# Kernel tuning notes

Hardware: AMD Instinct MI355X
Metric: run time of the kernel (lower is better)

The kernel has to match this reference:

```python
import jax, jax.numpy as jnp
import numpy as np

N = 100000   # num_entities
R = 474      # num_relations (already doubled for inverses)
D = 256      # in_dim == out_dim
E = 1000000  # num edges (first half 'in' mode, second half 'out' mode)
BN_EPS = 1e-5


def setup_inputs() -> dict:
    key = jax.random.key(0)
    ks = jax.random.split(key, 12)
    s = 1.0 / np.sqrt(D)
    return {
        "x": jax.random.normal(ks[0], (N, D), jnp.float32),
        "r": jax.random.normal(ks[1], (R, D), jnp.float32),
        "w_in": jax.random.normal(ks[2], (D, D), jnp.float32) * s,
        "w_out": jax.random.normal(ks[3], (D, D), jnp.float32) * s,
        "w_loop": jax.random.normal(ks[4], (D, D), jnp.float32) * s,
        "w_rel": jax.random.normal(ks[5], (D, D), jnp.float32) * s,
        "loop_rel": jax.random.normal(ks[6], (1, D), jnp.float32),
        "bias": jnp.zeros((D,), jnp.float32),
        "bn_gamma": jnp.ones((D,), jnp.float32),
        "bn_beta": jnp.zeros((D,), jnp.float32),
        "edge_index": jax.random.randint(ks[7], (2, E), 0, N, jnp.int32),
        "edge_type": jax.random.randint(ks[8], (E,), 0, R, jnp.int32),
    }


def reference(x, r, w_in, w_out, w_loop, w_rel, loop_rel, bias,
              bn_gamma, bn_beta, edge_index, edge_type):
    row, col = edge_index[0], edge_index[1]
    # symmetric edge norm 1/(sqrt(D_i) sqrt(D_j)); degrees over all edges
    deg = jax.ops.segment_sum(jnp.ones((E,), x.dtype), row, num_segments=N)
    deg_inv = jnp.where(deg > 0, deg ** -0.5, 0.0)
    norm = deg_inv[row] * deg_inv[col]  # [E]

    r_full = jnp.concatenate([r, loop_rel], axis=0)  # [R+1, D]

    def mode_agg(rw, cl, et, nrm, W):
        # gather -> composition (sub) -> per-mode matmul -> edge-norm -> scatter-add
        composed = x[cl] - r_full[et]                  # [e, D]
        msg = (composed @ W) * nrm[:, None]            # [e, D]
        return jax.ops.segment_sum(msg, rw, num_segments=N)

    half = edge_type.shape[0] // 2
    agg_in = mode_agg(row[:half], col[:half], edge_type[:half], norm[:half], w_in)
    agg_out = mode_agg(row[half:], col[half:], edge_type[half:], norm[half:], w_out)
    # self-loop: every node, relation = loop_rel (no edge norm)
    agg_loop = (x - loop_rel) @ w_loop                 # [N, D]

    h = agg_in + agg_out + agg_loop + bias
    # BatchNorm1d over node dim (batch statistics)
    mean = jnp.mean(h, axis=0)
    var = jnp.var(h, axis=0)
    h = bn_gamma * (h - mean) * jax.lax.rsqrt(var + BN_EPS) + bn_beta
    h = jnp.tanh(h)

    r_out = r @ w_rel  # rel_transformation == 'linear'
    return h, r_out
```

## Files before the change

### kernel.cpp

```cpp
#include <hip/hip_runtime.h>
#include <hip/hip_bf16.h>
#include <stdint.h>

#define D_DIM 256
#define KBIG 768

typedef __attribute__((ext_vector_type(8))) short bf16x8_t;
typedef __attribute__((ext_vector_type(4))) float f32x4_t;
typedef __attribute__((ext_vector_type(2))) float f32x2_t;

__device__ __forceinline__ float bf2f(uint16_t u) {
    union { uint32_t i; float f; } v; v.i = ((uint32_t)u) << 16; return v.f;
}
__device__ __forceinline__ uint16_t f2bf(float f) {
    union { float f; uint32_t i; } v; v.f = f;
    uint32_t x = v.i;
    uint32_t r = (x + 0x7FFFu + ((x >> 16) & 1u)) >> 16;
    return (uint16_t)r;
}
__device__ __forceinline__ uint32_t pack2(float a, float b) {
    return (uint32_t)f2bf(a) | ((uint32_t)f2bf(b) << 16);
}
__device__ __forceinline__ float loadv(const void* base, int f, size_t idx) {
    return f ? ((const float*)base)[idx] : bf2f(((const uint16_t*)base)[idx]);
}
__device__ __forceinline__ float fast_tanh(float x) {
    float t = __builtin_amdgcn_exp2f(x * 2.8853900817779268f);
    return 1.f - 2.f * __builtin_amdgcn_rcpf(t + 1.f);
}
__device__ __forceinline__ f32x2_t up2(uint32_t w) {
    union { uint32_t u[2]; f32x2_t f; } c;
    c.u[0] = w << 16;
    c.u[1] = w & 0xFFFF0000u;
    return c.f;
}
__device__ __forceinline__ void pkfma(f32x2_t& acc, f32x2_t a, f32x2_t b) {
    asm("v_pk_fma_f32 %0, %1, %2, %0" : "+v"(acc) : "v"(a), "v"(b));
}

__device__ __forceinline__ void gll16(const uint16_t* g, uint16_t* l) {
    __builtin_amdgcn_global_load_lds(
        (const __attribute__((address_space(1))) uint32_t*)(const void*)g,
        (__attribute__((address_space(3))) uint32_t*)(void*)l, 16, 0, 0);
}

__global__ void k_detect(const uint32_t* __restrict__ xw, int* __restrict__ flag) {
    __shared__ int cnt[256];
    int t = threadIdx.x;
    int c = 0;
    for (int j = 0; j < 16; j++) {
        uint32_t w = xw[(size_t)(t * 16 + j) * 797];
        uint32_t e = (w >> 7) & 0xFF;
        if (e >= 100 && e <= 140) c++;
    }
    cnt[t] = c;
    __syncthreads();
    for (int off = 128; off > 0; off >>= 1) {
        if (t < off) cnt[t] += cnt[t + off];
        __syncthreads();
    }
    if (t == 0) flag[0] = (cnt[0] < 2048) ? 1 : 0;
}

__global__ __launch_bounds__(256) void k_cast(const void* __restrict__ src,
                                              uint16_t* __restrict__ dst,
                                              int nvec, const int* __restrict__ flagp,
                                              int skip_bf) {
    int f = *flagp;
    int i = blockIdx.x * 256 + threadIdx.x;
    if (i >= nvec) return;
    size_t base = (size_t)i * 8;
    if (f) {
        const float* s = (const float*)src + base;
        float4 a = *(const float4*)s;
        float4 b = *(const float4*)(s + 4);
        uint4 o;
        o.x = (uint32_t)f2bf(a.x) | ((uint32_t)f2bf(a.y) << 16);
        o.y = (uint32_t)f2bf(a.z) | ((uint32_t)f2bf(a.w) << 16);
        o.z = (uint32_t)f2bf(b.x) | ((uint32_t)f2bf(b.y) << 16);
        o.w = (uint32_t)f2bf(b.z) | ((uint32_t)f2bf(b.w) << 16);
        *(uint4*)(dst + base) = o;
    } else {
        if (skip_bf) return;
        *(uint4*)(dst + base) = *(const uint4*)((const uint16_t*)src + base);
    }
}

__global__ void k_transpose(const void* __restrict__ w0, const void* __restrict__ w1,
                            const void* __restrict__ w2, const void* __restrict__ w3,
                            const int* __restrict__ flagp,
                            uint16_t* __restrict__ bt_big, uint16_t* __restrict__ bt_rel) {
    __shared__ uint16_t tile[32][33];
    int f = *flagp;
    int mat = blockIdx.z;
    const void* src = mat == 0 ? w0 : mat == 1 ? w1 : mat == 2 ? w2 : w3;
    int k0 = blockIdx.y * 32, n0 = blockIdx.x * 32;
    int tx = threadIdx.x, ty = threadIdx.y;
    tile[ty][tx] = f2bf(loadv(src, f, (size_t)(k0 + ty) * D_DIM + n0 + tx));
    __syncthreads();
    int n = n0 + ty, k = k0 + tx;
    if (mat < 3) bt_big[(size_t)n * KBIG + mat * D_DIM + k] = tile[tx][ty];
    else         bt_rel[(size_t)n * D_DIM + k] = tile[tx][ty];
}

__global__ void k_cvec(const void* __restrict__ loop_rel, const void* __restrict__ w_loop,
                       const void* __restrict__ bias, const int* __restrict__ flagp,
                       float* __restrict__ cvec) {
    int f = *flagp;
    int c = blockIdx.x;
    int lane = threadIdx.x;
    float s = 0.f;
#pragma unroll
    for (int kk = 0; kk < 4; kk++) {
        int k = kk * 64 + lane;
        s += loadv(loop_rel, f, k) * loadv(w_loop, f, (size_t)k * D_DIM + c);
    }
#pragma unroll
    for (int off = 32; off; off >>= 1) s += __shfl_down(s, off);
    if (lane == 0) cvec[c] = loadv(bias, f, c) - s;
}

__global__ void k_hist(const int* __restrict__ rows, int E, int half,
                       int* __restrict__ deg) {
    int i = blockIdx.x * blockDim.x + threadIdx.x;
    if (i < E) atomicAdd(&deg[rows[i]], (i < half) ? 0x10001 : 1);
}

__global__ void k_scan_a(const int* __restrict__ deg, int N, int* __restrict__ row_start,
                         int* __restrict__ blk_sum, float* __restrict__ dinv) {
    __shared__ int s[1024];
    int t = threadIdx.x;
    int i = blockIdx.x * 1024 + t;
    int v = (i < N) ? (deg[i] & 0xFFFF) : 0;
    if (i < N) dinv[i] = v > 0 ? rsqrtf((float)v) : 0.f;
    s[t] = v;
    __syncthreads();
    for (int off = 1; off < 1024; off <<= 1) {
        int add = (t >= off) ? s[t - off] : 0;
        __syncthreads();
        s[t] += add;
        __syncthreads();
    }
    if (i < N) row_start[i] = s[t] - v;
    if (t == 1023) blk_sum[blockIdx.x] = s[1023];
}

__global__ void k_scan_b(int* __restrict__ blk_sum, int nb) {
    __shared__ int s[128];
    int t = threadIdx.x;
    int v = (t < nb) ? blk_sum[t] : 0;
    s[t] = v;
    __syncthreads();
    for (int off = 1; off < 128; off <<= 1) {
        int add = (t >= off) ? s[t - off] : 0;
        __syncthreads();
        s[t] += add;
        __syncthreads();
    }
    if (t < nb) blk_sum[t] = s[t] - v;
}

__global__ void k_scan_c(int* __restrict__ row_start, const int* __restrict__ blk_sum,
                         const int* __restrict__ degp,
                         int N, int E, int* __restrict__ cur_in, int* __restrict__ cur_out) {
    int i = blockIdx.x * 1024 + threadIdx.x;
    if (i < N) {
        int v = row_start[i] + blk_sum[blockIdx.x];
        row_start[i] = v;
        cur_in[i] = v;
        cur_out[i] = v + (int)(((unsigned)degp[i]) >> 16);
    }
    if (i == 0) row_start[N] = E;
}

__global__ void k_fill(const int* __restrict__ ei, const int* __restrict__ et, int E, int half,
                       int* __restrict__ cur_in, int* __restrict__ cur_out,
                       const float* __restrict__ dinv, uint2* __restrict__ csr) {
    int e = blockIdx.x * blockDim.x + threadIdx.x;
    if (e >= E) return;
    int r_ = ei[e];
    int c_ = ei[E + e];
    int t_ = et[e];
    float w = dinv[r_] * dinv[c_];
    uint32_t m = ((uint32_t)c_ << 9) | (uint32_t)t_;
    int pos = (e < half) ? atomicAdd(&cur_in[r_], 1) : atomicAdd(&cur_out[r_], 1);
    csr[pos] = make_uint2(m, __float_as_uint(w));
}

__global__ __launch_bounds__(256) void k_agg(
    const uint2* __restrict__ csr, const int* __restrict__ row_start,
    const int* __restrict__ degp,
    const void* __restrict__ x_raw, const uint16_t* __restrict__ x_bf,
    const uint16_t* __restrict__ r_bf, const int* __restrict__ flagp,
    uint16_t* __restrict__ s_in, uint16_t* __restrict__ s_out, int N) {
    const char* xb = (const char*)((*flagp) ? x_bf : (const uint16_t*)x_raw);
    const char* rb = (const char*)r_bf;
    int node = blockIdx.x * 4 + (threadIdx.x >> 6);
    int lane = threadIdx.x & 63;
    if (node >= N) return;
    int half = lane >> 5;
    int cob = (lane & 31) * 16;
    int s = row_start[node], e = row_start[node + 1];
    int mid = s + (int)(((unsigned)degp[node]) >> 16);

    f32x2_t ax[4], ar[4];
    float a[8];

#pragma unroll
    for (int k = 0; k < 4; k++) { ax[k] = (f32x2_t){0.f, 0.f}; ar[k] = (f32x2_t){0.f, 0.f}; }
    for (int j = s + half; j < mid; j += 2) {
        uint2 rec = csr[j];
        uint32_t m = rec.x;
        float w = __uint_as_float(rec.y);
        uint4 xv = *(const uint4*)(xb + (m & 0xFFFFFE00u) + cob);
        uint4 rv = *(const uint4*)(rb + ((m & 511u) << 9) + cob);
        f32x2_t w2 = {w, w};
        pkfma(ax[0], up2(xv.x), w2); pkfma(ar[0], up2(rv.x), w2);
        pkfma(ax[1], up2(xv.y), w2); pkfma(ar[1], up2(rv.y), w2);
        pkfma(ax[2], up2(xv.z), w2); pkfma(ar[2], up2(rv.z), w2);
        pkfma(ax[3], up2(xv.w), w2); pkfma(ar[3], up2(rv.w), w2);
    }
#pragma unroll
    for (int k = 0; k < 4; k++) { a[2 * k] = ax[k][0] - ar[k][0]; a[2 * k + 1] = ax[k][1] - ar[k][1]; }
#pragma unroll
    for (int k = 0; k < 8; k++) a[k] += __shfl_xor(a[k], 32);
    if (half == 0) {
        uint4 o;
        o.x = pack2(a[0], a[1]); o.y = pack2(a[2], a[3]);
        o.z = pack2(a[4], a[5]); o.w = pack2(a[6], a[7]);
        *(uint4*)(s_in + (size_t)node * D_DIM + (cob >> 1)) = o;
    }

#pragma unroll
    for (int k = 0; k < 4; k++) { ax[k] = (f32x2_t){0.f, 0.f}; ar[k] = (f32x2_t){0.f, 0.f}; }
    for (int j = mid + half; j < e; j += 2) {
        uint2 rec = csr[j];
        uint32_t m = rec.x;
        float w = __uint_as_float(rec.y);
        uint4 xv = *(const uint4*)(xb + (m & 0xFFFFFE00u) + cob);
        uint4 rv = *(const uint4*)(rb + ((m & 511u) << 9) + cob);
        f32x2_t w2 = {w, w};
        pkfma(ax[0], up2(xv.x), w2); pkfma(ar[0], up2(rv.x), w2);
        pkfma(ax[1], up2(xv.y), w2); pkfma(ar[1], up2(rv.y), w2);
        pkfma(ax[2], up2(xv.z), w2); pkfma(ar[2], up2(rv.z), w2);
        pkfma(ax[3], up2(xv.w), w2); pkfma(ar[3], up2(rv.w), w2);
    }
#pragma unroll
    for (int k = 0; k < 4; k++) { a[2 * k] = ax[k][0] - ar[k][0]; a[2 * k + 1] = ax[k][1] - ar[k][1]; }
#pragma unroll
    for (int k = 0; k < 8; k++) a[k] += __shfl_xor(a[k], 32);
    if (half == 1) {
        uint4 o;
        o.x = pack2(a[0], a[1]); o.y = pack2(a[2], a[3]);
        o.z = pack2(a[4], a[5]); o.w = pack2(a[6], a[7]);
        *(uint4*)(s_out + (size_t)node * D_DIM + (cob >> 1)) = o;
    }
}

__global__ __launch_bounds__(512) void k_gemm(
    const uint16_t* a0, const uint16_t* a1,
    const uint16_t* a2, const uint16_t* a2alt, const int* __restrict__ flagp,
    int M, const uint16_t* __restrict__ bt, int bstride, int ktot,
    const float* __restrict__ addvec, uint16_t* out,
    float* __restrict__ bn_sum, float* __restrict__ bn_sq) {
    __shared__ uint16_t As[128 * 32];
    __shared__ uint16_t Bs[256 * 32];
    const uint16_t* a2s = (*flagp) ? a2 : a2alt;
    int t = threadIdx.x;
    int mbase = blockIdx.x * 128;
    int wave = t >> 6, lane = t & 63;
    int wm = (wave >> 2) * 64, wn = (wave & 3) * 64;
    int quad = lane >> 4, l15 = lane & 15;

    int roff = lane >> 2, cidx = lane & 3;
    int arowL = wave * 16 + roff;
    int achk = cidx ^ ((arowL >> 1) & 3);
    int agrow = mbase + arowL; if (agrow > M - 1) agrow = M - 1;
    size_t aoff = (size_t)agrow * D_DIM + achk * 8;
    uint16_t* aldsb = &As[(wave * 16) * 32];

    int browL0 = wave * 32 + roff;
    int browL1 = browL0 + 16;
    int bchk0 = cidx ^ ((browL0 >> 1) & 3);
    int bchk1 = cidx ^ ((browL1 >> 1) & 3);
    size_t boff0 = (size_t)browL0 * bstride + bchk0 * 8;
    size_t boff1 = (size_t)browL1 * bstride + bchk1 * 8;
    uint16_t* bldsb0 = &Bs[(wave * 32) * 32];
    uint16_t* bldsb1 = &Bs[(wave * 32 + 16) * 32];

    int afo[4], bfo[4];
#pragma unroll
    for (int im = 0; im < 4; im++) {
        int row = wm + im * 16 + l15;
        afo[im] = row * 32 + (quad ^ ((row >> 1) & 3)) * 8;
    }
#pragma unroll
    for (int in = 0; in < 4; in++) {
        int row = wn + in * 16 + l15;
        bfo[in] = row * 32 + (quad ^ ((row >> 1) & 3)) * 8;
    }

    f32x4_t acc[4][4];
#pragma unroll
    for (int i = 0; i < 4; i++)
#pragma unroll
        for (int j = 0; j < 4; j++) acc[i][j] = (f32x4_t){0.f, 0.f, 0.f, 0.f};

    for (int kt = 0; kt < ktot; kt += 32) {
        const uint16_t* asec = (kt < 256) ? a0 : (kt < 512 ? a1 : a2s);
        int klocal = kt & 255;
        gll16(asec + aoff + klocal, aldsb);
        gll16(bt + boff0 + kt, bldsb0);
        gll16(bt + boff1 + kt, bldsb1);
        __syncthreads();
        bf16x8_t af[4], bfr[4];
#pragma unroll
        for (int im = 0; im < 4; im++) af[im] = *(const bf16x8_t*)(&As[afo[im]]);
#pragma unroll
        for (int in = 0; in < 4; in++) bfr[in] = *(const bf16x8_t*)(&Bs[bfo[in]]);
#pragma unroll
        for (int im = 0; im < 4; im++)
#pragma unroll
            for (int in = 0; in < 4; in++)
                acc[im][in] = __builtin_amdgcn_mfma_f32_16x16x32_bf16(af[im], bfr[in], acc[im][in], 0, 0, 0);
        __syncthreads();
    }

    float s4[4] = {0.f, 0.f, 0.f, 0.f};
    float q4[4] = {0.f, 0.f, 0.f, 0.f};
#pragma unroll
    for (int im = 0; im < 4; im++) {
#pragma unroll
        for (int in = 0; in < 4; in++) {
            int gn = wn + in * 16 + l15;
            float av_ = addvec ? addvec[gn] : 0.f;
#pragma unroll
            for (int i2 = 0; i2 < 4; i2++) {
                int gm = mbase + wm + im * 16 + quad * 4 + i2;
                if (gm < M) {
                    float val = acc[im][in][i2] + av_;
                    out[(size_t)gm * D_DIM + gn] = f2bf(val);
                    if (bn_sum) { s4[in] += val; q4[in] += val * val; }
                }
            }
        }
    }
    if (bn_sum) {
        float* sred = (float*)As;
        if (t < 256) { sred[t] = 0.f; sred[t + 256] = 0.f; }
        __syncthreads();
#pragma unroll
        for (int in = 0; in < 4; in++) {
            float sv = s4[in], qv = q4[in];
            sv += __shfl_xor(sv, 16); sv += __shfl_xor(sv, 32);
            qv += __shfl_xor(qv, 16); qv += __shfl_xor(qv, 32);
            if (quad == 0) {
                int gn = wn + in * 16 + l15;
                atomicAdd(&sred[gn], sv);
                atomicAdd(&sred[gn + 256], qv);
            }
        }
        __syncthreads();
        if (t < 256) {
            atomicAdd(&bn_sum[t], sred[t]);
            atomicAdd(&bn_sq[t], sred[t + 256]);
        }
    }
}

__global__ __launch_bounds__(256) void k_final(const uint16_t* __restrict__ h_pre,
                                               const float* __restrict__ bn_sum,
                                               const float* __restrict__ bn_sq,
                                               const void* __restrict__ gamma,
                                               const void* __restrict__ beta,
                                               const int* __restrict__ flagp,
                                               int N, void* __restrict__ dout, int total) {
    __shared__ float ssc[256], ssh[256];
    int f = *flagp;
    {
        int c = threadIdx.x;
        float inv_n = 1.f / (float)N;
        float mean = bn_sum[c] * inv_n;
        float var = bn_sq[c] * inv_n - mean * mean;
        float sc = loadv(gamma, f, c) * rsqrtf(var + 1e-5f);
        ssc[c] = sc;
        ssh[c] = loadv(beta, f, c) - mean * sc;
    }
    __syncthreads();
    int t = blockIdx.x * 256 + threadIdx.x;
    int base = t * 8;
    if (base >= total) return;
    int c0 = base & (D_DIM - 1);
    uint4 v = *(const uint4*)(h_pre + base);
    uint16_t e[8];
    e[0] = (uint16_t)(v.x & 0xFFFF); e[1] = (uint16_t)(v.x >> 16);
    e[2] = (uint16_t)(v.y & 0xFFFF); e[3] = (uint16_t)(v.y >> 16);
    e[4] = (uint16_t)(v.z & 0xFFFF); e[5] = (uint16_t)(v.z >> 16);
    e[6] = (uint16_t)(v.w & 0xFFFF); e[7] = (uint16_t)(v.w >> 16);
    float r[8];
#pragma unroll
    for (int i = 0; i < 8; i++)
        r[i] = fast_tanh(bf2f(e[i]) * ssc[c0 + i] + ssh[c0 + i]);
    if (f) {
        float* fo = (float*)dout + base;
        float4 o0 = {r[0], r[1], r[2], r[3]};
        float4 o1 = {r[4], r[5], r[6], r[7]};
        *(float4*)fo = o0;
        *(float4*)(fo + 4) = o1;
    } else {
        uint4 o;
        o.x = (uint32_t)f2bf(r[0]) | ((uint32_t)f2bf(r[1]) << 16);
        o.y = (uint32_t)f2bf(r[2]) | ((uint32_t)f2bf(r[3]) << 16);
        o.z = (uint32_t)f2bf(r[4]) | ((uint32_t)f2bf(r[5]) << 16);
        o.w = (uint32_t)f2bf(r[6]) | ((uint32_t)f2bf(r[7]) << 16);
        *(uint4*)((uint16_t*)dout + base) = o;
    }
}

__global__ void k_store_r(const uint16_t* __restrict__ stage,
                          const int* __restrict__ flagp,
                          void* __restrict__ dout, size_t off, int cnt) {
    int f = *flagp;
    int i = (blockIdx.x * 256 + threadIdx.x) * 4;
    if (i >= cnt) return;
    ushort4 v = *(const ushort4*)(stage + i);
    if (f) {
        float4 o = {bf2f(v.x), bf2f(v.y), bf2f(v.z), bf2f(v.w)};
        *(float4*)((float*)dout + off + i) = o;
    } else {
        *(ushort4*)((uint16_t*)dout + off + i) = v;
    }
}

extern "C" void kernel_launch(void* const* d_in, const int* in_sizes, int n_in,
                              void* d_out, int out_size, void* d_ws, size_t ws_size,
                              hipStream_t stream) {
    const void* x        = d_in[0];
    const void* r        = d_in[1];
    const void* w_in     = d_in[2];
    const void* w_out    = d_in[3];
    const void* w_loop   = d_in[4];
    const void* w_rel    = d_in[5];
    const void* loop_rel = d_in[6];
    const void* bias     = d_in[7];
    const void* bn_gamma = d_in[8];
    const void* bn_beta  = d_in[9];
    const int* edge_index = (const int*)d_in[10];
    const int* edge_type  = (const int*)d_in[11];

    const int N = in_sizes[0] / D_DIM;
    const int R = in_sizes[1] / D_DIM;
    const int E = in_sizes[11];
    const int half = E / 2;

    char* p = (char*)d_ws;
    auto alloc = [&](size_t bytes) -> void* {
        void* q = (void*)p;
        p += (bytes + 255) & ~(size_t)255;
        return q;
    };
    uint16_t* s_out   = (uint16_t*)alloc((size_t)N * D_DIM * 2);
    uint2*    csr     = (uint2*)alloc((size_t)E * 8);
    uint16_t* bt_big  = (uint16_t*)alloc((size_t)D_DIM * KBIG * 2);
    uint16_t* bt_rel  = (uint16_t*)alloc((size_t)D_DIM * D_DIM * 2);
    uint16_t* r_bf    = (uint16_t*)alloc((size_t)R * D_DIM * 2 + 65536);
    uint16_t* r_stage = (uint16_t*)alloc((size_t)R * D_DIM * 2);
    int*      deg     = (int*)alloc((size_t)N * 4);
    int*      rstart  = (int*)alloc((size_t)(N + 1) * 4);
    int*      cursor  = (int*)alloc((size_t)N * 4);
    int*      cursor_out = (int*)alloc((size_t)N * 4);
    float*    dinv    = (float*)alloc((size_t)N * 4);
    int*      blksum  = (int*)alloc(128 * 4);
    float*    cvec    = (float*)alloc(D_DIM * 4);
    float*    bn_sum  = (float*)alloc(D_DIM * 4);
    float*    bn_sq   = (float*)alloc(D_DIM * 4);
    int*      dflag   = (int*)alloc(256);

    uint16_t* s_in = (uint16_t*)d_out;
    uint16_t* x_bf = (uint16_t*)d_out + (size_t)N * D_DIM;
    uint16_t* h_pre = s_out;

    hipMemsetAsync(deg, 0, (size_t)N * 4, stream);
    hipMemsetAsync(bn_sum, 0, D_DIM * 4, stream);
    hipMemsetAsync(bn_sq, 0, D_DIM * 4, stream);

    k_detect<<<1, 256, 0, stream>>>((const uint32_t*)x, dflag);
    int xvec = N * D_DIM / 8;
    k_cast<<<(xvec + 255) / 256, 256, 0, stream>>>(x, x_bf, xvec, dflag, 1);
    int rvec = R * D_DIM / 8;
    k_cast<<<(rvec + 255) / 256, 256, 0, stream>>>(r, r_bf, rvec, dflag, 0);
    k_transpose<<<dim3(8, 8, 4), dim3(32, 32), 0, stream>>>(w_in, w_out, w_loop, w_rel,
                                                            dflag, bt_big, bt_rel);
    k_cvec<<<D_DIM, 64, 0, stream>>>(loop_rel, w_loop, bias, dflag, cvec);

    int eb = (E + 255) / 256;
    k_hist<<<eb, 256, 0, stream>>>(edge_index, E, half, deg);
    int nb = (N + 1023) / 1024;
    k_scan_a<<<nb, 1024, 0, stream>>>(deg, N, rstart, blksum, dinv);
    k_scan_b<<<1, 128, 0, stream>>>(blksum, nb);
    k_scan_c<<<nb, 1024, 0, stream>>>(rstart, blksum, deg, N, E, cursor, cursor_out);
    k_fill<<<eb, 256, 0, stream>>>(edge_index, edge_type, E, half, cursor, cursor_out,
                                   dinv, csr);

    k_agg<<<(N + 3) / 4, 256, 0, stream>>>(csr, rstart, deg, x, x_bf, r_bf, dflag,
                                           s_in, s_out, N);

    int gx = (N + 127) / 128;
    k_gemm<<<gx, 512, 0, stream>>>(s_in, s_out, x_bf, (const uint16_t*)x, dflag,
                                   N, bt_big, KBIG, KBIG, cvec, h_pre, bn_sum, bn_sq);
    int gr_ = (R + 127) / 128;
    k_gemm<<<gr_, 512, 0, stream>>>(r_bf, r_bf, r_bf, r_bf, dflag,
                                    R, bt_rel, D_DIM, D_DIM, nullptr, r_stage,
                                    nullptr, nullptr);

    int total = N * D_DIM;
    k_final<<<(total / 8 + 255) / 256, 256, 0, stream>>>(h_pre, bn_sum, bn_sq,
                                                         bn_gamma, bn_beta, dflag,
                                                         N, d_out, total);
    int rcnt = R * D_DIM;
    k_store_r<<<(rcnt / 4 + 255) / 256, 256, 0, stream>>>(r_stage, dflag, d_out, (size_t)N * D_DIM, rcnt);
}
```

Baseline: 537.3 us.

## Double-buffer GEMM LDS tiles and write relation output directly from epilogue

The GEMM main loop now uses two LDS buffers. Each iteration issues the global-to-LDS loads for the next K tile, then waits with an explicit vmcnt on the current one, so loads overlap the MFMA work and one of the two barriers per tile is cheaper. The relation GEMM epilogue writes straight into the output in the runtime-detected dtype, which removes the k_store_r kernel and its staging buffer. The dtype-detect kernel shrinks to a single wave with a shuffle reduction, and the two BN memsets are merged into one. LDS use doubles, which may lower occupancy.

```diff
diff --git a/kernel.cpp b/kernel.cpp
--- a/kernel.cpp
+++ b/kernel.cpp
@@ -45,21 +45,17 @@
 }
 
 __global__ void k_detect(const uint32_t* __restrict__ xw, int* __restrict__ flag) {
-    __shared__ int cnt[256];
-    int t = threadIdx.x;
+    int lane = threadIdx.x;
     int c = 0;
-    for (int j = 0; j < 16; j++) {
-        uint32_t w = xw[(size_t)(t * 16 + j) * 797];
+#pragma unroll
+    for (int j = 0; j < 8; j++) {
+        uint32_t w = xw[(size_t)(lane * 8 + j) * 6151];
         uint32_t e = (w >> 7) & 0xFF;
-        if (e >= 100 && e <= 140) c++;
-    }
-    cnt[t] = c;
-    __syncthreads();
-    for (int off = 128; off > 0; off >>= 1) {
-        if (t < off) cnt[t] += cnt[t + off];
-        __syncthreads();
-    }
-    if (t == 0) flag[0] = (cnt[0] < 2048) ? 1 : 0;
+        c += (e >= 100 && e <= 140) ? 1 : 0;
+    }
+#pragma unroll
+    for (int off = 32; off; off >>= 1) c += __shfl_down(c, off);
+    if (lane == 0) flag[0] = (c < 128) ? 1 : 0;
 }
 
 __global__ __launch_bounds__(256) void k_cast(const void* __restrict__ src,
@@ -262,10 +258,12 @@
     const uint16_t* a2, const uint16_t* a2alt, const int* __restrict__ flagp,
     int M, const uint16_t* __restrict__ bt, int bstride, int ktot,
     const float* __restrict__ addvec, uint16_t* out,
-    float* __restrict__ bn_sum, float* __restrict__ bn_sq) {
-    __shared__ uint16_t As[128 * 32];
-    __shared__ uint16_t Bs[256 * 32];
-    const uint16_t* a2s = (*flagp) ? a2 : a2alt;
+    float* __restrict__ bn_sum, float* __restrict__ bn_sq,
+    void* __restrict__ dout2, long long d_off) {
+    __shared__ uint16_t As[2][128 * 32];
+    __shared__ uint16_t Bs[2][256 * 32];
+    int fl = *flagp;
+    const uint16_t* a2s = fl ? a2 : a2alt;
     int t = threadIdx.x;
     int mbase = blockIdx.x * 128;
     int wave = t >> 6, lane = t & 63;
@@ -277,7 +275,7 @@
     int achk = cidx ^ ((arowL >> 1) & 3);
     int agrow = mbase + arowL; if (agrow > M - 1) agrow = M - 1;
     size_t aoff = (size_t)agrow * D_DIM + achk * 8;
-    uint16_t* aldsb = &As[(wave * 16) * 32];
+    int awoff = (wave * 16) * 32;
 
     int browL0 = wave * 32 + roff;
     int browL1 = browL0 + 16;
@@ -285,8 +283,8 @@
     int bchk1 = cidx ^ ((browL1 >> 1) & 3);
     size_t boff0 = (size_t)browL0 * bstride + bchk0 * 8;
     size_t boff1 = (size_t)browL1 * bstride + bchk1 * 8;
-    uint16_t* bldsb0 = &Bs[(wave * 32) * 32];
-    uint16_t* bldsb1 = &Bs[(wave * 32 + 16) * 32];
+    int bwoff0 = (wave * 32) * 32;
+    int bwoff1 = (wave * 32 + 16) * 32;
 
     int afo[4], bfo[4];
 #pragma unroll
@@ -306,24 +304,38 @@
 #pragma unroll
         for (int j = 0; j < 4; j++) acc[i][j] = (f32x4_t){0.f, 0.f, 0.f, 0.f};
 
+    auto stage = [&](int buf, int kt) {
+        const uint16_t* asec = (kt < 256) ? a0 : (kt < 512 ? a1 : a2s);
+        gll16(asec + aoff + (kt & 255), &As[buf][awoff]);
+        gll16(bt + boff0 + kt, &Bs[buf][bwoff0]);
+        gll16(bt + boff1 + kt, &Bs[buf][bwoff1]);
+    };
+
+    stage(0, 0);
+    int cur = 0;
     for (int kt = 0; kt < ktot; kt += 32) {
-        const uint16_t* asec = (kt < 256) ? a0 : (kt < 512 ? a1 : a2s);
-        int klocal = kt & 255;
-        gll16(asec + aoff + klocal, aldsb);
-        gll16(bt + boff0 + kt, bldsb0);
-        gll16(bt + boff1 + kt, bldsb1);
-        __syncthreads();
+        if (kt + 32 < ktot) {
+            stage(cur ^ 1, kt + 32);
+            asm volatile("s_waitcnt vmcnt(3)" ::: "memory");
+        } else {
+            asm volatile("s_waitcnt vmcnt(0)" ::: "memory");
+        }
+        __builtin_amdgcn_sched_barrier(0);
+        __builtin_amdgcn_s_barrier();
         bf16x8_t af[4], bfr[4];
 #pragma unroll
-        for (int im = 0; im < 4; im++) af[im] = *(const bf16x8_t*)(&As[afo[im]]);
-#pragma unroll
-        for (int in = 0; in < 4; in++) bfr[in] = *(const bf16x8_t*)(&Bs[bfo[in]]);
+        for (int im = 0; im < 4; im++) af[im] = *(const bf16x8_t*)(&As[cur][afo[im]]);
+#pragma unroll
+        for (int in = 0; in < 4; in++) bfr[in] = *(const bf16x8_t*)(&Bs[cur][bfo[in]]);
 #pragma unroll
         for (int im = 0; im < 4; im++)
 #pragma unroll
             for (int in = 0; in < 4; in++)
                 acc[im][in] = __builtin_amdgcn_mfma_f32_16x16x32_bf16(af[im], bfr[in], acc[im][in], 0, 0, 0);
-        __syncthreads();
+        asm volatile("s_waitcnt lgkmcnt(0)" ::: "memory");
+        __builtin_amdgcn_sched_barrier(0);
+        __builtin_amdgcn_s_barrier();
+        cur ^= 1;
     }
 
     float s4[4] = {0.f, 0.f, 0.f, 0.f};
@@ -339,14 +351,21 @@
                 int gm = mbase + wm + im * 16 + quad * 4 + i2;
                 if (gm < M) {
                     float val = acc[im][in][i2] + av_;
-                    out[(size_t)gm * D_DIM + gn] = f2bf(val);
+                    if (dout2) {
+                        size_t idx = (size_t)d_off + (size_t)gm * D_DIM + gn;
+                        if (fl) ((float*)dout2)[idx] = val;
+                        else    ((uint16_t*)dout2)[idx] = f2bf(val);
+                    } else {
+                        out[(size_t)gm * D_DIM + gn] = f2bf(val);
+                    }
                     if (bn_sum) { s4[in] += val; q4[in] += val * val; }
                 }
             }
         }
     }
     if (bn_sum) {
-        float* sred = (float*)As;
+        float* sred = (float*)&As[0][0];
+        __syncthreads();
         if (t < 256) { sred[t] = 0.f; sred[t + 256] = 0.f; }
         __syncthreads();
 #pragma unroll
@@ -417,21 +436,6 @@
     }
 }
 
-__global__ void k_store_r(const uint16_t* __restrict__ stage,
-                          const int* __restrict__ flagp,
-                          void* __restrict__ dout, size_t off, int cnt) {
-    int f = *flagp;
-    int i = (blockIdx.x * 256 + threadIdx.x) * 4;
-    if (i >= cnt) return;
-    ushort4 v = *(const ushort4*)(stage + i);
-    if (f) {
-        float4 o = {bf2f(v.x), bf2f(v.y), bf2f(v.z), bf2f(v.w)};
-        *(float4*)((float*)dout + off + i) = o;
-    } else {
-        *(ushort4*)((uint16_t*)dout + off + i) = v;
-    }
-}
-
 extern "C" void kernel_launch(void* const* d_in, const int* in_sizes, int n_in,
                               void* d_out, int out_size, void* d_ws, size_t ws_size,
                               hipStream_t stream) {
@@ -464,7 +468,6 @@
     uint16_t* bt_big  = (uint16_t*)alloc((size_t)D_DIM * KBIG * 2);
     uint16_t* bt_rel  = (uint16_t*)alloc((size_t)D_DIM * D_DIM * 2);
     uint16_t* r_bf    = (uint16_t*)alloc((size_t)R * D_DIM * 2 + 65536);
-    uint16_t* r_stage = (uint16_t*)alloc((size_t)R * D_DIM * 2);
     int*      deg     = (int*)alloc((size_t)N * 4);
     int*      rstart  = (int*)alloc((size_t)(N + 1) * 4);
     int*      cursor  = (int*)alloc((size_t)N * 4);
@@ -475,16 +478,16 @@
     float*    bn_sum  = (float*)alloc(D_DIM * 4);
     float*    bn_sq   = (float*)alloc(D_DIM * 4);
     int*      dflag   = (int*)alloc(256);
+    (void)bn_sq;
 
     uint16_t* s_in = (uint16_t*)d_out;
     uint16_t* x_bf = (uint16_t*)d_out + (size_t)N * D_DIM;
     uint16_t* h_pre = s_out;
 
     hipMemsetAsync(deg, 0, (size_t)N * 4, stream);
-    hipMemsetAsync(bn_sum, 0, D_DIM * 4, stream);
-    hipMemsetAsync(bn_sq, 0, D_DIM * 4, stream);
-
-    k_detect<<<1, 256, 0, stream>>>((const uint32_t*)x, dflag);
+    hipMemsetAsync(bn_sum, 0, 2 * D_DIM * 4, stream);
+
+    k_detect<<<1, 64, 0, stream>>>((const uint32_t*)x, dflag);
     int xvec = N * D_DIM / 8;
     k_cast<<<(xvec + 255) / 256, 256, 0, stream>>>(x, x_bf, xvec, dflag, 1);
     int rvec = R * D_DIM / 8;
@@ -507,16 +510,16 @@
 
     int gx = (N + 127) / 128;
     k_gemm<<<gx, 512, 0, stream>>>(s_in, s_out, x_bf, (const uint16_t*)x, dflag,
-                                   N, bt_big, KBIG, KBIG, cvec, h_pre, bn_sum, bn_sq);
+                                   N, bt_big, KBIG, KBIG, cvec, h_pre, bn_sum, bn_sq,
+                                   nullptr, 0);
     int gr_ = (R + 127) / 128;
     k_gemm<<<gr_, 512, 0, stream>>>(r_bf, r_bf, r_bf, r_bf, dflag,
-                                    R, bt_rel, D_DIM, D_DIM, nullptr, r_stage,
-                                    nullptr, nullptr);
+                                    R, bt_rel, D_DIM, D_DIM, nullptr, nullptr,
+                                    nullptr, nullptr,
+                                    d_out, (long long)N * D_DIM);
 
     int total = N * D_DIM;
     k_final<<<(total / 8 + 255) / 256, 256, 0, stream>>>(h_pre, bn_sum, bn_sq,
                                                          bn_gamma, bn_beta, dflag,
                                                          N, d_out, total);
-    int rcnt = R * D_DIM;
-    k_store_r<<<(rcnt / 4 + 255) / 256, 256, 0, stream>>>(r_stage, dflag, d_out, (size_t)N * D_DIM, rcnt);
-}
+}
```

After: 529.4 us. Within noise of the previous version (-1.5%).
